# Optimization experiments

Measured on AMD Instinct MI355X. Metric: run time of the kernel, lower is better.

The kernel has to match this reference:

```python
import jax, jax.numpy as jnp
import numpy as np

N = 320   # batch of events
D = 64    # features per event
P = 1000  # permutation_count (hard-coded in module)


def setup_inputs() -> dict:
    key = jax.random.key(0)
    k1, k2, k3 = jax.random.split(key, 3)
    data = jax.random.normal(k1, (N, D), dtype=jnp.float32)
    particle_types = jax.random.randint(k2, (N,), 0, 2, dtype=jnp.int32)
    # quantum permutations: 1000 independent random permutations of [0, N)
    perms = jax.vmap(lambda k: jax.random.permutation(k, N))(jax.random.split(k3, P)).astype(jnp.int32)
    return {
        "data": data,
        "fermion_antisymmetry": jnp.float32(-1.0),
        "boson_symmetry": jnp.float32(1.0),
        "particle_types": particle_types,
        "perms": perms,
    }


def reference(data, fermion_antisymmetry, boson_symmetry, particle_types, perms):
    n = data.shape[0]
    tf = particle_types  # [n]
    # statistics factor matrix F[i,j]: fermion-fermion -> -1 param, boson-boson -> +1 param, mixed -> 1.0
    ff = (tf[:, None] == 0) & (tf[None, :] == 0)
    bb = (tf[:, None] == 1) & (tf[None, :] == 1)
    F = jnp.where(ff, fermion_antisymmetry, jnp.where(bb, boson_symmetry, jnp.float32(1.0)))  # [n,n]

    ar = jnp.arange(n)
    gathered = data[perms]                      # [P,n,d] = data[perm[i]]
    fac = F[ar[None, :], perms]                 # [P,n]   = F[i, perm[i]]
    same = perms == ar[None, :]                 # i == perm[i]: keep original row unscaled
    perm_data = jnp.where(same[..., None], gathered, fac[..., None] * gathered)  # [P,n,d]

    all_data = jnp.concatenate([data[None], perm_data], axis=0)  # [P+1,n,d]; row 0 = original

    # pairwise Euclidean norms via Gram trick (avoids [P+1,n,n,d] diff tensor)
    sn = jnp.sum(all_data * all_data, axis=-1)                   # [P+1,n]
    gram = jnp.einsum('pnd,pmd->pnm', all_data, all_data)        # [P+1,n,n]
    sq = jnp.maximum(sn[:, :, None] + sn[:, None, :] - 2.0 * gram, 0.0)

    iu, ju = jnp.triu_indices(n, k=1)
    vals = F[iu, ju][None, :] * jnp.sqrt(sq[:, iu, ju])          # [P+1, n*(n-1)/2]
    # torch.var default is unbiased (ddof=1)
    stats = jnp.var(vals, axis=1, ddof=1)                        # [P+1]
    return stats  # stats[0] = original test statistic, stats[1:] = permutation null distribution
```

## Files before the change

kernel.cpp:

```cpp
#include <hip/hip_runtime.h>
#include <math.h>

#define NN 320
#define DD 64
#define NPERM 1001
#define KPB 4
#define NBLK ((NPERM + KPB - 1) / KPB)
#define NW 10
#define NPAIRF ((double)(NN * (NN - 1) / 2))


__global__ __launch_bounds__(NN) void dah_kernel(const float* __restrict__ data,
                                                 float2* __restrict__ DAH,
                                                 double* __restrict__ srow,
                                                 double* __restrict__ rsda) {
    __shared__ float rowa[DD];
    __shared__ double cr[5];
    const int a = blockIdx.x;
    const int t = threadIdx.x;
    if (t < DD) rowa[t] = data[a * DD + t];
    __syncthreads();
    const float* rb = data + t * DD;
    float g = 0.f, sa = 0.f, st = 0.f;
#pragma unroll
    for (int k = 0; k < DD; k += 4) {
        const float4 x = *(const float4*)(rb + k);
        const float r0 = rowa[k], r1 = rowa[k + 1], r2 = rowa[k + 2], r3 = rowa[k + 3];
        g  = fmaf(r0, x.x, g);   g  = fmaf(r1, x.y, g);
        g  = fmaf(r2, x.z, g);   g  = fmaf(r3, x.w, g);
        sa = fmaf(r0, r0, sa);   sa = fmaf(r1, r1, sa);
        sa = fmaf(r2, r2, sa);   sa = fmaf(r3, r3, sa);
        st = fmaf(x.x, x.x, st); st = fmaf(x.y, x.y, st);
        st = fmaf(x.z, x.z, st); st = fmaf(x.w, x.w, st);
    }
    const float sum = sa + st;
    const float dp = sqrtf(fmaxf(fmaf(-2.f, g, sum), 0.f));
    const float dm = sqrtf(fmaxf(fmaf( 2.f, g, sum), 0.f));
    const float da = 0.5f * (dp + dm);
    const float dh = 0.5f * (dp - dm);
    DAH[(size_t)a * NN + t] = make_float2(da, dh);

    double cd = (double)da;
    for (int off = 32; off; off >>= 1) cd += __shfl_down(cd, off, 64);
    const int wid = t >> 6, lane = t & 63;
    if (lane == 0) cr[wid] = cd;
    __syncthreads();
    if (t == 0) {
        double tot = 0.0;
#pragma unroll
        for (int i = 0; i < 5; ++i) tot += cr[i];
        rsda[a] = tot;
        srow[a] = (double)sa;
    }
}

__global__ __launch_bounds__(512, 2) void qf_kernel(const float* __restrict__ data,
                                                    const int* __restrict__ types,
                                                    const int* __restrict__ perms,
                                                    const float* __restrict__ fermp,
                                                    const float* __restrict__ bosp,
                                                    const float* __restrict__ DAHf,
                                                    const double* __restrict__ srow,
                                                    const double* __restrict__ rsda,
                                                    float* __restrict__ out) {
    __shared__ unsigned cb[KPB][2 * NW];
    __shared__ __align__(16) float rcoef[NN * 5 * 4];
    __shared__ float ysh[KPB][2][DD];
    __shared__ double red[8][12];
    __shared__ double redS[8], redC[8], scal[KPB];

    const int pg = blockIdx.x;
    const int t  = threadIdx.x;

    if (t < KPB * 2 * NW) ((unsigned*)cb)[t] = 0u;
    __syncthreads();
    const float Fv = *fermp, Bv = *bosp;
    if (t < NN) {
        const int i  = t;
        const int ti = types[i];
#pragma unroll
        for (int k = 0; k < KPB; ++k) {
            int p = pg * KPB + k; if (p >= NPERM) p = NPERM - 1;
            const int a  = (p == 0) ? i : perms[(size_t)(p - 1) * NN + i];
            const int ta = types[a];
            float u = 1.f;
            if (a != i) u = (ti == 0 && ta == 0) ? Fv : ((ti == 1 && ta == 1) ? Bv : 1.f);
            if (u < 0.f) atomicOr(&cb[k][a >> 5], 1u << (a & 31));
            if (ti == 0) atomicOr(&cb[k][NW + (a >> 5)], 1u << (a & 31));
        }
    }
    __syncthreads();

    for (int j = t; j < NN * KPB; j += 512) {
        const int r = j >> 2, k = j & 3;
        const unsigned ubit = (cb[k][r >> 5]        >> (r & 31)) & 1u;
        const unsigned qbit = (cb[k][NW + (r >> 5)] >> (r & 31)) & 1u;
        const float u = ubit ? -1.f : 1.f;
        *(float4*)&rcoef[(r * 5 + k) * 4] =
            make_float4(u, qbit ? 1.f : 0.f, qbit ? u : 0.f, 0.f);
    }

    const int strip  = t % 40;
    const int rowoff = t / 40;
    const int col0   = strip * 8;
    float ub[KPB][8], qb[KPB][8], vb[KPB][8];
    if (rowoff < 12) {
#pragma unroll
        for (int k = 0; k < KPB; ++k) {
            const unsigned uw = cb[k][col0 >> 5]        >> (col0 & 31);
            const unsigned qw = cb[k][NW + (col0 >> 5)] >> (col0 & 31);
#pragma unroll
            for (int e = 0; e < 8; ++e) {
                const float u = ((uw >> e) & 1u) ? -1.f : 1.f;
                const bool  q = ((qw >> e) & 1u) != 0u;
                ub[k][e] = u;
                qb[k][e] = q ? 1.f : 0.f;
                vb[k][e] = q ? u : 0.f;
            }
        }
    }
    __syncthreads();

    float A2[KPB] = {0.f, 0.f, 0.f, 0.f};
    float A3[KPB] = {0.f, 0.f, 0.f, 0.f};
    float A4[KPB] = {0.f, 0.f, 0.f, 0.f};

    if (rowoff < 12) {
        const int STRIDE = 12 * NN * 2;
        const float* gp  = DAHf + (size_t)(rowoff * NN + col0) * 2;
        const float* app = rcoef + rowoff * 20;
        float4 c0 = *(const float4*)(gp);
        float4 c1 = *(const float4*)(gp + 4);
        float4 c2 = *(const float4*)(gp + 8);
        float4 c3 = *(const float4*)(gp + 12);

        auto compute = [&](const float* ap) {
#pragma unroll
            for (int k = 0; k < KPB; ++k) {
                const float4 rp = *(const float4*)(ap + k * 4);
                float r2 = ub[k][0] * c0.y;
                float r3 = qb[k][0] * c0.x;
                float r4 = vb[k][0] * c0.y;
                r2 = fmaf(ub[k][1], c0.w, r2); r3 = fmaf(qb[k][1], c0.z, r3); r4 = fmaf(vb[k][1], c0.w, r4);
                r2 = fmaf(ub[k][2], c1.y, r2); r3 = fmaf(qb[k][2], c1.x, r3); r4 = fmaf(vb[k][2], c1.y, r4);
                r2 = fmaf(ub[k][3], c1.w, r2); r3 = fmaf(qb[k][3], c1.z, r3); r4 = fmaf(vb[k][3], c1.w, r4);
                r2 = fmaf(ub[k][4], c2.y, r2); r3 = fmaf(qb[k][4], c2.x, r3); r4 = fmaf(vb[k][4], c2.y, r4);
                r2 = fmaf(ub[k][5], c2.w, r2); r3 = fmaf(qb[k][5], c2.z, r3); r4 = fmaf(vb[k][5], c2.w, r4);
                r2 = fmaf(ub[k][6], c3.y, r2); r3 = fmaf(qb[k][6], c3.x, r3); r4 = fmaf(vb[k][6], c3.y, r4);
                r2 = fmaf(ub[k][7], c3.w, r2); r3 = fmaf(qb[k][7], c3.z, r3); r4 = fmaf(vb[k][7], c3.w, r4);
                A2[k] = fmaf(rp.x, r2, A2[k]);
                A3[k] = fmaf(rp.y, r3, A3[k]);
                A4[k] = fmaf(rp.z, r4, A4[k]);
            }
        };

#pragma unroll 2
        for (int it = 0; it < 26; ++it) {
            const float* gq = gp + STRIDE;
            if (it == 25 && rowoff >= 8) gq = gp;
            const float4 n0 = *(const float4*)(gq);
            const float4 n1 = *(const float4*)(gq + 4);
            const float4 n2 = *(const float4*)(gq + 8);
            const float4 n3 = *(const float4*)(gq + 12);
            compute(app);
            c0 = n0; c1 = n1; c2 = n2; c3 = n3;
            gp = gq; app += 240;
        }
        if (rowoff < 8) compute(app);
    }

    {
        const int k = t >> 7, sub = t & 127;
        const int j = sub >> 6, d = sub & 63;
        float acc = 0.f;
        const int r0 = j * (NN / 2);
        for (int r = r0; r < r0 + NN / 2; ++r)
            acc = fmaf(rcoef[(r * 5 + k) * 4], data[(size_t)r * DD + d], acc);
        ysh[k][j][d] = acc;
    }

    double rd[12];
#pragma unroll
    for (int k = 0; k < KPB; ++k) {
        rd[k]     = (double)A2[k];
        rd[4 + k] = (double)A3[k];
        rd[8 + k] = (double)A4[k];
    }
    for (int off = 32; off; off >>= 1) {
#pragma unroll
        for (int j = 0; j < 12; ++j) rd[j] += __shfl_down(rd[j], off, 64);
    }
    const int wid = t >> 6, lane = t & 63;
    if (lane == 0) {
#pragma unroll
        for (int j = 0; j < 12; ++j) red[wid][j] = rd[j];
    }

    {
        double sS = 0.0, sC = 0.0;
        if (t < NN) { sS = srow[t]; sC = rsda[t]; }
        for (int off = 32; off; off >>= 1) {
            sS += __shfl_down(sS, off, 64);
            sC += __shfl_down(sC, off, 64);
        }
        if (lane == 0) { redS[wid] = sS; redC[wid] = sC; }
    }
    __syncthreads();

    if (t < KPB * 64) {
        const int k = t >> 6, d = t & 63;
        const float yv = ysh[k][0][d] + ysh[k][1][d];
        double yy = (double)yv * (double)yv;
        for (int off = 32; off; off >>= 1) yy += __shfl_down(yy, off, 64);
        if ((t & 63) == 0) scal[k] = yy;
    }
    __syncthreads();

    if (t == 0) {
        double S = 0.0, C0 = 0.0;
#pragma unroll
        for (int w = 0; w < 8; ++w) { S += redS[w]; C0 += redC[w]; }
#pragma unroll
        for (int k = 0; k < KPB; ++k) {
            const int p = pg * KPB + k;
            if (p < NPERM) {
                double T2 = 0.0, T3 = 0.0, T4 = 0.0;
#pragma unroll
                for (int w = 0; w < 8; ++w) {
                    T2 += red[w][k];
                    T3 += red[w][4 + k];
                    T4 += red[w][8 + k];
                }
                const double SV  = 0.5 * (C0 + T2 - 2.0 * T3 - 2.0 * T4);
                const double SV2 = (double)NN * S - scal[k];
                out[p] = (float)((SV2 - SV * SV / NPAIRF) / (NPAIRF - 1.0));
            }
        }
    }
}

extern "C" void kernel_launch(void* const* d_in, const int* in_sizes, int n_in,
                              void* d_out, int out_size, void* d_ws, size_t ws_size,
                              hipStream_t stream) {
    const float* data  = (const float*)d_in[0];
    const float* fermp = (const float*)d_in[1];
    const float* bosp  = (const float*)d_in[2];
    const int*   types = (const int*)d_in[3];
    const int*   perms = (const int*)d_in[4];
    float* out = (float*)d_out;

    double* srow = (double*)d_ws;
    double* rsda = (double*)((char*)d_ws + 4096);
    float2* DAH  = (float2*)((char*)d_ws + 1048576);

    dah_kernel<<<NN, NN, 0, stream>>>(data, DAH, srow, rsda);
    qf_kernel<<<NBLK, 512, 0, stream>>>(data, types, perms, fermp, bosp,
                                        (const float*)DAH, srow, rsda, out);
}
```

Measured before the change: 94.29 us.

## Stage DAH panels through double-buffered LDS with register prefetch in qf_kernel

The main accumulation loop in qf_kernel now copies 16-row panels of the DAH matrix into a double-buffered shared-memory array. The copy uses coalesced float4 loads, and the next panel is prefetched into registers one step ahead. Threads are remapped to 64 strips by 8 row offsets, each handling 5 columns spaced 64 apart, so all 512 threads do equal work instead of 480 with a ragged tail. The aim is better global-load coalescing and latency hiding. The cost is an extra LDS round trip, about 100KB of shared memory, a barrier per panel, and dropping the 2-blocks-per-CU launch hint.

New measurement: 127.5 us. 35.2% more time.

```diff
diff --git a/kernel.cpp b/kernel.cpp
--- a/kernel.cpp
+++ b/kernel.cpp
@@ -7,6 +7,9 @@
 #define KPB 4
 #define NBLK ((NPERM + KPB - 1) / KPB)
 #define NW 10
+#define PROWS 16
+#define NPANEL (NN / PROWS)
+#define PANEL_F4 (PROWS * NN * 2 / 4)
 #define NPAIRF ((double)(NN * (NN - 1) / 2))
 
 
@@ -54,23 +57,26 @@
     }
 }
 
-__global__ __launch_bounds__(512, 2) void qf_kernel(const float* __restrict__ data,
-                                                    const int* __restrict__ types,
-                                                    const int* __restrict__ perms,
-                                                    const float* __restrict__ fermp,
-                                                    const float* __restrict__ bosp,
-                                                    const float* __restrict__ DAHf,
-                                                    const double* __restrict__ srow,
-                                                    const double* __restrict__ rsda,
-                                                    float* __restrict__ out) {
+__global__ __launch_bounds__(512) void qf_kernel(const float* __restrict__ data,
+                                                 const int* __restrict__ types,
+                                                 const int* __restrict__ perms,
+                                                 const float* __restrict__ fermp,
+                                                 const float* __restrict__ bosp,
+                                                 const float* __restrict__ DAHf,
+                                                 const double* __restrict__ srow,
+                                                 const double* __restrict__ rsda,
+                                                 float* __restrict__ out) {
+    __shared__ float buf[2][PROWS * NN * 2];
     __shared__ unsigned cb[KPB][2 * NW];
-    __shared__ __align__(16) float rcoef[NN * 5 * 4];
+    __shared__ __align__(16) float rcoef[NN * 20];
     __shared__ float ysh[KPB][2][DD];
     __shared__ double red[8][12];
     __shared__ double redS[8], redC[8], scal[KPB];
 
     const int pg = blockIdx.x;
     const int t  = threadIdx.x;
+    const int strip  = t & 63;
+    const int rowoff = t >> 6;
 
     if (t < KPB * 2 * NW) ((unsigned*)cb)[t] = 0u;
     __syncthreads();
@@ -91,6 +97,11 @@
     }
     __syncthreads();
 
+    const float4* dall = (const float4*)DAHf;
+    float4 stg[5];
+#pragma unroll
+    for (int j = 0; j < 5; ++j) stg[j] = dall[t + 512 * j];
+
     for (int j = t; j < NN * KPB; j += 512) {
         const int r = j >> 2, k = j & 3;
         const unsigned ubit = (cb[k][r >> 5]        >> (r & 31)) & 1u;
@@ -100,24 +111,26 @@
             make_float4(u, qbit ? 1.f : 0.f, qbit ? u : 0.f, 0.f);
     }
 
-    const int strip  = t % 40;
-    const int rowoff = t / 40;
-    const int col0   = strip * 8;
-    float ub[KPB][8], qb[KPB][8], vb[KPB][8];
-    if (rowoff < 12) {
-#pragma unroll
-        for (int k = 0; k < KPB; ++k) {
-            const unsigned uw = cb[k][col0 >> 5]        >> (col0 & 31);
-            const unsigned qw = cb[k][NW + (col0 >> 5)] >> (col0 & 31);
-#pragma unroll
-            for (int e = 0; e < 8; ++e) {
-                const float u = ((uw >> e) & 1u) ? -1.f : 1.f;
-                const bool  q = ((qw >> e) & 1u) != 0u;
-                ub[k][e] = u;
-                qb[k][e] = q ? 1.f : 0.f;
-                vb[k][e] = q ? u : 0.f;
-            }
-        }
+    float ub[KPB][5], qb[KPB][5], vb[KPB][5];
+#pragma unroll
+    for (int k = 0; k < KPB; ++k) {
+#pragma unroll
+        for (int e = 0; e < 5; ++e) {
+            const int w = (strip >> 5) + 2 * e, b = strip & 31;
+            const float u = ((cb[k][w] >> b) & 1u) ? -1.f : 1.f;
+            const bool  q = ((cb[k][NW + w] >> b) & 1u) != 0u;
+            ub[k][e] = u;
+            qb[k][e] = q ? 1.f : 0.f;
+            vb[k][e] = q ? u : 0.f;
+        }
+    }
+
+    {
+        float4* db = (float4*)buf[0];
+#pragma unroll
+        for (int j = 0; j < 5; ++j) db[t + 512 * j] = stg[j];
+#pragma unroll
+        for (int j = 0; j < 5; ++j) stg[j] = dall[PANEL_F4 + t + 512 * j];
     }
     __syncthreads();
 
@@ -125,48 +138,45 @@
     float A3[KPB] = {0.f, 0.f, 0.f, 0.f};
     float A4[KPB] = {0.f, 0.f, 0.f, 0.f};
 
-    if (rowoff < 12) {
-        const int STRIDE = 12 * NN * 2;
-        const float* gp  = DAHf + (size_t)(rowoff * NN + col0) * 2;
-        const float* app = rcoef + rowoff * 20;
-        float4 c0 = *(const float4*)(gp);
-        float4 c1 = *(const float4*)(gp + 4);
-        float4 c2 = *(const float4*)(gp + 8);
-        float4 c3 = *(const float4*)(gp + 12);
-
-        auto compute = [&](const float* ap) {
-#pragma unroll
-            for (int k = 0; k < KPB; ++k) {
-                const float4 rp = *(const float4*)(ap + k * 4);
-                float r2 = ub[k][0] * c0.y;
-                float r3 = qb[k][0] * c0.x;
-                float r4 = vb[k][0] * c0.y;
-                r2 = fmaf(ub[k][1], c0.w, r2); r3 = fmaf(qb[k][1], c0.z, r3); r4 = fmaf(vb[k][1], c0.w, r4);
-                r2 = fmaf(ub[k][2], c1.y, r2); r3 = fmaf(qb[k][2], c1.x, r3); r4 = fmaf(vb[k][2], c1.y, r4);
-                r2 = fmaf(ub[k][3], c1.w, r2); r3 = fmaf(qb[k][3], c1.z, r3); r4 = fmaf(vb[k][3], c1.w, r4);
-                r2 = fmaf(ub[k][4], c2.y, r2); r3 = fmaf(qb[k][4], c2.x, r3); r4 = fmaf(vb[k][4], c2.y, r4);
-                r2 = fmaf(ub[k][5], c2.w, r2); r3 = fmaf(qb[k][5], c2.z, r3); r4 = fmaf(vb[k][5], c2.w, r4);
-                r2 = fmaf(ub[k][6], c3.y, r2); r3 = fmaf(qb[k][6], c3.x, r3); r4 = fmaf(vb[k][6], c3.y, r4);
-                r2 = fmaf(ub[k][7], c3.w, r2); r3 = fmaf(qb[k][7], c3.z, r3); r4 = fmaf(vb[k][7], c3.w, r4);
-                A2[k] = fmaf(rp.x, r2, A2[k]);
-                A3[k] = fmaf(rp.y, r3, A3[k]);
-                A4[k] = fmaf(rp.z, r4, A4[k]);
-            }
-        };
-
-#pragma unroll 2
-        for (int it = 0; it < 26; ++it) {
-            const float* gq = gp + STRIDE;
-            if (it == 25 && rowoff >= 8) gq = gp;
-            const float4 n0 = *(const float4*)(gq);
-            const float4 n1 = *(const float4*)(gq + 4);
-            const float4 n2 = *(const float4*)(gq + 8);
-            const float4 n3 = *(const float4*)(gq + 12);
-            compute(app);
-            c0 = n0; c1 = n1; c2 = n2; c3 = n3;
-            gp = gq; app += 240;
-        }
-        if (rowoff < 8) compute(app);
+    auto row_compute = [&](const float* rowp, const float* ap) {
+        const float2 m0 = *(const float2*)(rowp + 2 * strip);
+        const float2 m1 = *(const float2*)(rowp + 2 * strip + 128);
+        const float2 m2 = *(const float2*)(rowp + 2 * strip + 256);
+        const float2 m3 = *(const float2*)(rowp + 2 * strip + 384);
+        const float2 m4 = *(const float2*)(rowp + 2 * strip + 512);
+#pragma unroll
+        for (int k = 0; k < KPB; ++k) {
+            const float4 rp = *(const float4*)(ap + 4 * k);
+            float r2 = ub[k][0] * m0.y;
+            float r3 = qb[k][0] * m0.x;
+            float r4 = vb[k][0] * m0.y;
+            r2 = fmaf(ub[k][1], m1.y, r2); r3 = fmaf(qb[k][1], m1.x, r3); r4 = fmaf(vb[k][1], m1.y, r4);
+            r2 = fmaf(ub[k][2], m2.y, r2); r3 = fmaf(qb[k][2], m2.x, r3); r4 = fmaf(vb[k][2], m2.y, r4);
+            r2 = fmaf(ub[k][3], m3.y, r2); r3 = fmaf(qb[k][3], m3.x, r3); r4 = fmaf(vb[k][3], m3.y, r4);
+            r2 = fmaf(ub[k][4], m4.y, r2); r3 = fmaf(qb[k][4], m4.x, r3); r4 = fmaf(vb[k][4], m4.y, r4);
+            A2[k] = fmaf(rp.x, r2, A2[k]);
+            A3[k] = fmaf(rp.y, r3, A3[k]);
+            A4[k] = fmaf(rp.z, r4, A4[k]);
+        }
+    };
+
+    for (int p = 0; p < NPANEL; ++p) {
+        if (p + 1 < NPANEL) {
+            float4* db = (float4*)buf[(p + 1) & 1];
+#pragma unroll
+            for (int j = 0; j < 5; ++j) db[t + 512 * j] = stg[j];
+        }
+        if (p + 2 < NPANEL) {
+#pragma unroll
+            for (int j = 0; j < 5; ++j)
+                stg[j] = dall[(size_t)(p + 2) * PANEL_F4 + t + 512 * j];
+        }
+        const float* B = buf[p & 1];
+        row_compute(B + rowoff * (2 * NN),
+                    rcoef + (p * PROWS + rowoff) * 20);
+        row_compute(B + (rowoff + 8) * (2 * NN),
+                    rcoef + (p * PROWS + rowoff + 8) * 20);
+        if (p + 1 < NPANEL) __syncthreads();
     }
 
     {
```

## Fuse distance precompute and permutation kernels via cooperative grid sync

Applied to the files above, without the earlier changes.

Merges the pairwise distance precompute kernel into the main permutation kernel. Each of the 251 blocks computes one or two rows of DAH, then all blocks meet at a cooperative grid sync, which removes one kernel launch and the gap between kernels. The DAH streaming loop also moves from a one-stage to a two-stage register prefetch. The cost is a grid-wide barrier, a cooperative launch whose grid must be fully co-resident, and more register pressure from the extra prefetch buffers.

After: 164.7 us. 1.75x slower.

```diff
diff --git a/kernel.cpp b/kernel.cpp
--- a/kernel.cpp
+++ b/kernel.cpp
@@ -1,5 +1,8 @@
 #include <hip/hip_runtime.h>
+#include <hip/hip_cooperative_groups.h>
 #include <math.h>
+
+namespace cg = cooperative_groups;
 
 #define NN 320
 #define DD 64
@@ -10,67 +13,77 @@
 #define NPAIRF ((double)(NN * (NN - 1) / 2))
 
 
-__global__ __launch_bounds__(NN) void dah_kernel(const float* __restrict__ data,
-                                                 float2* __restrict__ DAH,
-                                                 double* __restrict__ srow,
-                                                 double* __restrict__ rsda) {
+__global__ __launch_bounds__(512, 2)
+void fused_kernel(const float* __restrict__ data,
+                  const int* __restrict__ types,
+                  const int* __restrict__ perms,
+                  const float* __restrict__ fermp,
+                  const float* __restrict__ bosp,
+                  void* __restrict__ ws,
+                  float* __restrict__ out) {
+    double* srow = (double*)ws;
+    double* rsda = (double*)((char*)ws + 4096);
+    float2* DAH  = (float2*)((char*)ws + 1048576);
+    const float* DAHf = (const float*)DAH;
+
     __shared__ float rowa[DD];
     __shared__ double cr[5];
-    const int a = blockIdx.x;
-    const int t = threadIdx.x;
-    if (t < DD) rowa[t] = data[a * DD + t];
-    __syncthreads();
-    const float* rb = data + t * DD;
-    float g = 0.f, sa = 0.f, st = 0.f;
-#pragma unroll
-    for (int k = 0; k < DD; k += 4) {
-        const float4 x = *(const float4*)(rb + k);
-        const float r0 = rowa[k], r1 = rowa[k + 1], r2 = rowa[k + 2], r3 = rowa[k + 3];
-        g  = fmaf(r0, x.x, g);   g  = fmaf(r1, x.y, g);
-        g  = fmaf(r2, x.z, g);   g  = fmaf(r3, x.w, g);
-        sa = fmaf(r0, r0, sa);   sa = fmaf(r1, r1, sa);
-        sa = fmaf(r2, r2, sa);   sa = fmaf(r3, r3, sa);
-        st = fmaf(x.x, x.x, st); st = fmaf(x.y, x.y, st);
-        st = fmaf(x.z, x.z, st); st = fmaf(x.w, x.w, st);
-    }
-    const float sum = sa + st;
-    const float dp = sqrtf(fmaxf(fmaf(-2.f, g, sum), 0.f));
-    const float dm = sqrtf(fmaxf(fmaf( 2.f, g, sum), 0.f));
-    const float da = 0.5f * (dp + dm);
-    const float dh = 0.5f * (dp - dm);
-    DAH[(size_t)a * NN + t] = make_float2(da, dh);
-
-    double cd = (double)da;
-    for (int off = 32; off; off >>= 1) cd += __shfl_down(cd, off, 64);
-    const int wid = t >> 6, lane = t & 63;
-    if (lane == 0) cr[wid] = cd;
-    __syncthreads();
-    if (t == 0) {
-        double tot = 0.0;
-#pragma unroll
-        for (int i = 0; i < 5; ++i) tot += cr[i];
-        rsda[a] = tot;
-        srow[a] = (double)sa;
-    }
-}
-
-__global__ __launch_bounds__(512, 2) void qf_kernel(const float* __restrict__ data,
-                                                    const int* __restrict__ types,
-                                                    const int* __restrict__ perms,
-                                                    const float* __restrict__ fermp,
-                                                    const float* __restrict__ bosp,
-                                                    const float* __restrict__ DAHf,
-                                                    const double* __restrict__ srow,
-                                                    const double* __restrict__ rsda,
-                                                    float* __restrict__ out) {
     __shared__ unsigned cb[KPB][2 * NW];
-    __shared__ __align__(16) float rcoef[NN * 5 * 4];
+    __shared__ __align__(16) float rcoef[NN * 20];
     __shared__ float ysh[KPB][2][DD];
     __shared__ double red[8][12];
     __shared__ double redS[8], redC[8], scal[KPB];
 
+    const int t = threadIdx.x;
+
+#pragma unroll
+    for (int rr = 0; rr < 2; ++rr) {
+        const int a = blockIdx.x + rr * NBLK;
+        if (a < NN) {
+            if (t < DD) rowa[t] = data[a * DD + t];
+            __syncthreads();
+            if (t < NN) {
+                const float* rb = data + t * DD;
+                float g = 0.f, sa = 0.f, st = 0.f;
+#pragma unroll
+                for (int k = 0; k < DD; k += 4) {
+                    const float4 x = *(const float4*)(rb + k);
+                    const float r0 = rowa[k], r1 = rowa[k + 1];
+                    const float r2 = rowa[k + 2], r3 = rowa[k + 3];
+                    g  = fmaf(r0, x.x, g);   g  = fmaf(r1, x.y, g);
+                    g  = fmaf(r2, x.z, g);   g  = fmaf(r3, x.w, g);
+                    sa = fmaf(r0, r0, sa);   sa = fmaf(r1, r1, sa);
+                    sa = fmaf(r2, r2, sa);   sa = fmaf(r3, r3, sa);
+                    st = fmaf(x.x, x.x, st); st = fmaf(x.y, x.y, st);
+                    st = fmaf(x.z, x.z, st); st = fmaf(x.w, x.w, st);
+                }
+                const float sum = sa + st;
+                const float dp = sqrtf(fmaxf(fmaf(-2.f, g, sum), 0.f));
+                const float dm = sqrtf(fmaxf(fmaf( 2.f, g, sum), 0.f));
+                const float da = 0.5f * (dp + dm);
+                const float dh = 0.5f * (dp - dm);
+                DAH[(size_t)a * NN + t] = make_float2(da, dh);
+
+                double cd = (double)da;
+                for (int off = 32; off; off >>= 1) cd += __shfl_down(cd, off, 64);
+                if ((t & 63) == 0) cr[t >> 6] = cd;
+                if (t == 0) srow[a] = (double)sa;
+            }
+            __syncthreads();
+            if (t == 0) {
+                double tot = 0.0;
+#pragma unroll
+                for (int i = 0; i < 5; ++i) tot += cr[i];
+                rsda[a] = tot;
+            }
+            __syncthreads();
+        }
+    }
+
+    __threadfence();
+    cg::this_grid().sync();
+
     const int pg = blockIdx.x;
-    const int t  = threadIdx.x;
 
     if (t < KPB * 2 * NW) ((unsigned*)cb)[t] = 0u;
     __syncthreads();
@@ -126,28 +139,35 @@
     float A4[KPB] = {0.f, 0.f, 0.f, 0.f};
 
     if (rowoff < 12) {
-        const int STRIDE = 12 * NN * 2;
-        const float* gp  = DAHf + (size_t)(rowoff * NN + col0) * 2;
-        const float* app = rcoef + rowoff * 20;
-        float4 c0 = *(const float4*)(gp);
-        float4 c1 = *(const float4*)(gp + 4);
-        float4 c2 = *(const float4*)(gp + 8);
-        float4 c3 = *(const float4*)(gp + 12);
-
-        auto compute = [&](const float* ap) {
+        const size_t STRIDE = (size_t)12 * NN * 2;
+        const float* base = DAHf + (size_t)(rowoff * NN + col0) * 2;
+        const float* app  = rcoef + rowoff * 20;
+
+        float4 a0, a1, a2, a3, b0, b1, b2, b3;
+        {
+            const float* g0 = base;
+            a0 = *(const float4*)(g0);      a1 = *(const float4*)(g0 + 4);
+            a2 = *(const float4*)(g0 + 8);  a3 = *(const float4*)(g0 + 12);
+            const float* g1 = base + STRIDE;
+            b0 = *(const float4*)(g1);      b1 = *(const float4*)(g1 + 4);
+            b2 = *(const float4*)(g1 + 8);  b3 = *(const float4*)(g1 + 12);
+        }
+
+        auto compute = [&](const float4& d0, const float4& d1,
+                           const float4& d2, const float4& d3, const float* ap) {
 #pragma unroll
             for (int k = 0; k < KPB; ++k) {
-                const float4 rp = *(const float4*)(ap + k * 4);
-                float r2 = ub[k][0] * c0.y;
-                float r3 = qb[k][0] * c0.x;
-                float r4 = vb[k][0] * c0.y;
-                r2 = fmaf(ub[k][1], c0.w, r2); r3 = fmaf(qb[k][1], c0.z, r3); r4 = fmaf(vb[k][1], c0.w, r4);
-                r2 = fmaf(ub[k][2], c1.y, r2); r3 = fmaf(qb[k][2], c1.x, r3); r4 = fmaf(vb[k][2], c1.y, r4);
-                r2 = fmaf(ub[k][3], c1.w, r2); r3 = fmaf(qb[k][3], c1.z, r3); r4 = fmaf(vb[k][3], c1.w, r4);
-                r2 = fmaf(ub[k][4], c2.y, r2); r3 = fmaf(qb[k][4], c2.x, r3); r4 = fmaf(vb[k][4], c2.y, r4);
-                r2 = fmaf(ub[k][5], c2.w, r2); r3 = fmaf(qb[k][5], c2.z, r3); r4 = fmaf(vb[k][5], c2.w, r4);
-                r2 = fmaf(ub[k][6], c3.y, r2); r3 = fmaf(qb[k][6], c3.x, r3); r4 = fmaf(vb[k][6], c3.y, r4);
-                r2 = fmaf(ub[k][7], c3.w, r2); r3 = fmaf(qb[k][7], c3.z, r3); r4 = fmaf(vb[k][7], c3.w, r4);
+                const float4 rp = *(const float4*)(ap + 4 * k);
+                float r2 = ub[k][0] * d0.y;
+                float r3 = qb[k][0] * d0.x;
+                float r4 = vb[k][0] * d0.y;
+                r2 = fmaf(ub[k][1], d0.w, r2); r3 = fmaf(qb[k][1], d0.z, r3); r4 = fmaf(vb[k][1], d0.w, r4);
+                r2 = fmaf(ub[k][2], d1.y, r2); r3 = fmaf(qb[k][2], d1.x, r3); r4 = fmaf(vb[k][2], d1.y, r4);
+                r2 = fmaf(ub[k][3], d1.w, r2); r3 = fmaf(qb[k][3], d1.z, r3); r4 = fmaf(vb[k][3], d1.w, r4);
+                r2 = fmaf(ub[k][4], d2.y, r2); r3 = fmaf(qb[k][4], d2.x, r3); r4 = fmaf(vb[k][4], d2.y, r4);
+                r2 = fmaf(ub[k][5], d2.w, r2); r3 = fmaf(qb[k][5], d2.z, r3); r4 = fmaf(vb[k][5], d2.w, r4);
+                r2 = fmaf(ub[k][6], d3.y, r2); r3 = fmaf(qb[k][6], d3.x, r3); r4 = fmaf(vb[k][6], d3.y, r4);
+                r2 = fmaf(ub[k][7], d3.w, r2); r3 = fmaf(qb[k][7], d3.z, r3); r4 = fmaf(vb[k][7], d3.w, r4);
                 A2[k] = fmaf(rp.x, r2, A2[k]);
                 A3[k] = fmaf(rp.y, r3, A3[k]);
                 A4[k] = fmaf(rp.z, r4, A4[k]);
@@ -156,17 +176,18 @@
 
 #pragma unroll 2
         for (int it = 0; it < 26; ++it) {
-            const float* gq = gp + STRIDE;
-            if (it == 25 && rowoff >= 8) gq = gp;
-            const float4 n0 = *(const float4*)(gq);
-            const float4 n1 = *(const float4*)(gq + 4);
-            const float4 n2 = *(const float4*)(gq + 8);
-            const float4 n3 = *(const float4*)(gq + 12);
-            compute(app);
-            c0 = n0; c1 = n1; c2 = n2; c3 = n3;
-            gp = gq; app += 240;
-        }
-        if (rowoff < 8) compute(app);
+            const int pf = it + 2;
+            const int pfc = (pf < 26 || (pf == 26 && rowoff < 8)) ? pf : it;
+            const float* g2 = base + (size_t)pfc * STRIDE;
+            const float4 c0v = *(const float4*)(g2);
+            const float4 c1v = *(const float4*)(g2 + 4);
+            const float4 c2v = *(const float4*)(g2 + 8);
+            const float4 c3v = *(const float4*)(g2 + 12);
+            compute(a0, a1, a2, a3, app + it * 240);
+            a0 = b0; a1 = b1; a2 = b2; a3 = b3;
+            b0 = c0v; b1 = c1v; b2 = c2v; b3 = c3v;
+        }
+        if (rowoff < 8) compute(a0, a1, a2, a3, app + 26 * 240);
     }
 
     {
@@ -248,12 +269,10 @@
     const int*   types = (const int*)d_in[3];
     const int*   perms = (const int*)d_in[4];
     float* out = (float*)d_out;
-
-    double* srow = (double*)d_ws;
-    double* rsda = (double*)((char*)d_ws + 4096);
-    float2* DAH  = (float2*)((char*)d_ws + 1048576);
-
-    dah_kernel<<<NN, NN, 0, stream>>>(data, DAH, srow, rsda);
-    qf_kernel<<<NBLK, 512, 0, stream>>>(data, types, perms, fermp, bosp,
-                                        (const float*)DAH, srow, rsda, out);
+    void*  ws  = d_ws;
+
+    void* args[] = { (void*)&data, (void*)&types, (void*)&perms,
+                     (void*)&fermp, (void*)&bosp, (void*)&ws, (void*)&out };
+    hipLaunchCooperativeKernel((const void*)fused_kernel,
+                               dim3(NBLK), dim3(512), args, 0, stream);
 }
```
